# Kernel tuning notes

Measured on AMD Instinct MI355X. Metric: run time of the kernel, lower is better.

Reference implementation:

```python
import jax, jax.numpy as jnp
import numpy as np


def setup_inputs() -> dict:
    key = jax.random.key(0)
    k1, k2, k3 = jax.random.split(key, 3)
    B, C, H, W = 8, 256, 64, 64
    l = jax.random.normal(k1, (B, C, H, W), dtype=jnp.float32)
    # 1x1 conv weights [out=C//2, in=C]; scale 1/sqrt(C) so projected features have ~unit variance
    scale = 1.0 / np.sqrt(C)
    w_theta = jax.random.normal(k2, (C // 2, C), dtype=jnp.float32) * scale
    w_phi = jax.random.normal(k3, (C // 2, C), dtype=jnp.float32) * scale
    return {"l": l, "w_theta": w_theta, "w_phi": w_phi}


def reference(l, w_theta, w_phi):
    # NonLocalOp forward with embed=True, softmax=True
    B, C, H, W = l.shape
    E = w_theta.shape[0]  # C // 2
    HW = H * W
    # 1x1 convs == per-pixel linear maps
    theta = jnp.einsum('bchw,ec->behw', l, w_theta).reshape(B, E, HW)  # [B,E,HW]
    phi = jnp.einsum('bchw,ec->behw', l, w_phi).reshape(B, E, HW)      # [B,E,HW]
    g = l.reshape(B, C, HW)                                            # [B,C,HW]
    # scores: theta^T phi over embed channels, scaled by sqrt(C//2)
    scale = 1.0 / jnp.sqrt(jnp.asarray(C // 2, dtype=l.dtype))
    f = jnp.einsum('beq,bek->bqk', theta, phi) * scale                 # [B,HW,HW]
    f = jax.nn.softmax(f, axis=-1)
    out = jnp.einsum('bqk,bck->bcq', f, g).reshape(B, C, H, W)
    return out
```

## Files before the change

kernel.cpp:

```cpp
#include <hip/hip_runtime.h>
#include <stdint.h>

#define NB 8
#define NC 256
#define NE 128
#define NHW 4096

typedef __bf16 v8bf __attribute__((ext_vector_type(8)));
typedef float v4f __attribute__((ext_vector_type(4)));
typedef float v16f __attribute__((ext_vector_type(16)));
typedef unsigned int v4u __attribute__((ext_vector_type(4)));

typedef unsigned int __attribute__((address_space(1))) uint_g;
typedef unsigned int __attribute__((address_space(3))) uint_l;

#if __has_builtin(__builtin_amdgcn_exp2f)
#define EXP2F(x) __builtin_amdgcn_exp2f(x)
#else
#define EXP2F(x) exp2f(x)
#endif

#define BARRIER_LDS() asm volatile("s_waitcnt lgkmcnt(0)\n\ts_barrier" ::: "memory")
#define WAIT_VM0()    asm volatile("s_waitcnt vmcnt(0)" ::: "memory")

__device__ __forceinline__ void dma16(const unsigned short* g, unsigned short* l) {
    __builtin_amdgcn_global_load_lds((const uint_g*)g, (uint_l*)l, 16, 0, 0);
}

__device__ __forceinline__ unsigned short f2bf(float x) {
    union { float f; unsigned int u; } v; v.f = x;
    unsigned int r = v.u + 0x7fffu + ((v.u >> 16) & 1u);
    return (unsigned short)(r >> 16);
}

__device__ __forceinline__ unsigned int pack_bf2_ru(float a, float b) {
    union { float f; unsigned int u; } va, vb; va.f = a; vb.f = b;
    return ((va.u + 0x8000u) >> 16) | ((vb.u + 0x8000u) & 0xffff0000u);
}

__global__ __launch_bounds__(256) void cast_w_kernel(const float* __restrict__ wt,
                                                     const float* __restrict__ wp,
                                                     unsigned short* __restrict__ Wbf) {
    int i = blockIdx.x * 256 + threadIdx.x;
    const float QS = 0.08838834764831845f * 1.4426950408889634f;
    float v = (i < 32768) ? wt[i] * QS : wp[i - 32768];
    Wbf[i] = f2bf(v);
}

__global__ __launch_bounds__(256, 2) void proj_kernel(const float* __restrict__ l,
                                                      const unsigned short* __restrict__ Wbf,
                                                      unsigned short* __restrict__ Qbf,
                                                      unsigned short* __restrict__ Kbf,
                                                      unsigned short* __restrict__ Vbf) {
    __shared__ __align__(16) unsigned short A[64][264];
    __shared__ __align__(16) unsigned short Ost[2][32][136];
    const int tid = threadIdx.x;
    const int b = blockIdx.x & 7;
    const int qt = (blockIdx.x >> 3) << 6;
    const float* lb = l + ((size_t)b * NC * NHW + qt);

    for (int s = 0; s < 16; ++s) {
        int f = tid + s * 256;
        int c = f >> 4, j = f & 15;
        float4 v = *(const float4*)(lb + (size_t)c * NHW + j * 4);
        ushort4 o4;
        o4.x = f2bf(v.x); o4.y = f2bf(v.y); o4.z = f2bf(v.z); o4.w = f2bf(v.w);
        A[j * 4 + 0][c] = o4.x;
        A[j * 4 + 1][c] = o4.y;
        A[j * 4 + 2][c] = o4.z;
        A[j * 4 + 3][c] = o4.w;
        *(ushort4*)(Vbf + (size_t)b * NC * NHW + (size_t)c * NHW + qt + j * 4) = o4;
    }
    __syncthreads();

    const int w = tid >> 6, L = tid & 63;
    const int l15 = L & 15, q4 = L >> 4;
    const v4f vz = {0.f, 0.f, 0.f, 0.f};
    v4f acc[4][4];
    for (int mt = 0; mt < 4; ++mt)
        for (int nt = 0; nt < 4; ++nt) acc[mt][nt] = vz;

    for (int kf = 0; kf < 8; ++kf) {
        int kc = kf * 32 + q4 * 8;
        v8bf a[4], bb[4];
        for (int mt = 0; mt < 4; ++mt)
            a[mt] = *(const v8bf*)&A[mt * 16 + l15][kc];
        for (int nt = 0; nt < 4; ++nt)
            bb[nt] = *(const v8bf*)(Wbf + (w * 64 + nt * 16 + l15) * 256 + kc);
        for (int mt = 0; mt < 4; ++mt)
            for (int nt = 0; nt < 4; ++nt)
                acc[mt][nt] = __builtin_amdgcn_mfma_f32_16x16x32_bf16(a[mt], bb[nt], acc[mt][nt], 0, 0, 0);
    }

    const int side = w >> 1;
    const int ebase = (w & 1) * 64;
#pragma unroll
    for (int ph = 0; ph < 2; ++ph) {
        __syncthreads();
#pragma unroll
        for (int mh = 0; mh < 2; ++mh) {
            int mt = ph * 2 + mh;
#pragma unroll
            for (int nt = 0; nt < 4; ++nt)
#pragma unroll
                for (int r = 0; r < 4; ++r) {
                    int q32 = mh * 16 + q4 * 4 + r;
                    Ost[side][q32][ebase + nt * 16 + l15] = f2bf(acc[mt][nt][r]);
                }
        }
        __syncthreads();
#pragma unroll
        for (int s = 0; s < 4; ++s) {
            int idx = tid + s * 256;
            int sd = idx >> 9, rem = idx & 511;
            int r32 = rem >> 4, c8 = rem & 15;
            unsigned short* dst = sd ? Kbf : Qbf;
            int c8s = sd ? (c8 ^ (r32 & 15)) : c8;
            *(uint4*)(dst + ((size_t)b * NHW + qt + ph * 32 + r32) * NE + c8s * 8) =
                *(const uint4*)&Ost[sd][r32][c8 * 8];
        }
    }
}

__global__ __launch_bounds__(512, 2) void attn_kernel(const unsigned short* __restrict__ Qbf,
                                                      const unsigned short* __restrict__ Kbf,
                                                      const unsigned short* __restrict__ Vbf,
                                                      float* __restrict__ out) {
    __shared__ __align__(16) unsigned char smem[66048];
    unsigned short* KuS = (unsigned short*)smem;
    unsigned short* PuS = (unsigned short*)(smem + 32768);
    float* lsumF = (float*)(smem + 65536);

    const int tid = threadIdx.x;
    const int b = blockIdx.x & 7;
    const int q128 = (blockIdx.x >> 3) << 7;
    const int w = tid >> 6;
    const int L = tid & 63;
    const int l31 = L & 31, hi = L >> 5;
    const int x15 = l31 & 15;

    const unsigned short* Kb = Kbf + (size_t)b * NHW * NE;
    const unsigned short* Vb = Vbf + (size_t)b * NC * NHW;

    v16f o[2][4];
#pragma unroll
    for (int ct = 0; ct < 2; ++ct)
#pragma unroll
        for (int qt = 0; qt < 4; ++qt)
#pragma unroll
            for (int r = 0; r < 16; ++r) o[ct][qt][r] = 0.f;
    float lacc = 0.f;

    v8bf bq[8];
    v8bf av[2][4];
    const unsigned short* vb0 = nullptr;
    const unsigned short* vb1 = nullptr;

    if (w < 4) {
        const unsigned short* qrow = Qbf + ((size_t)b * NHW + q128 + w * 32 + l31) * NE + hi * 8;
#pragma unroll
        for (int ef = 0; ef < 8; ++ef)
            bq[ef] = *(const v8bf*)(qrow + ef * 16);
#pragma unroll
        for (int jj = 0; jj < 4; ++jj) {
            int j = w * 4 + jj;
            dma16(Kb + (size_t)j * 512 + L * 8, KuS + j * 512);
        }
        WAIT_VM0();
    } else {
        int ci = w - 4;
        vb0 = Vb + (size_t)(ci * 64 + l31) * NHW + hi * 8;
        vb1 = Vb + (size_t)(ci * 64 + 32 + l31) * NHW + hi * 8;
#pragma unroll
        for (int kf = 0; kf < 4; ++kf) {
            av[0][kf] = *(const v8bf*)(vb0 + kf * 16);
            av[1][kf] = *(const v8bf*)(vb1 + kf * 16);
        }
    }
    BARRIER_LDS();

    for (int it = 0; it < 65; ++it) {
        if (w < 4 && it < 64) {
            const int buf = it & 1;
            const int nbuf = (it + 1) & 1;
            const size_t ktn = (size_t)((it + 1) & 63) * 64;
#pragma unroll
            for (int jj = 0; jj < 4; ++jj) {
                int j = w * 4 + jj;
                dma16(Kb + ktn * NE + (size_t)j * 512 + L * 8, KuS + nbuf * 8192 + j * 512);
            }
            const unsigned short* kub = KuS + buf * 8192;
#pragma unroll
            for (int kt = 0; kt < 2; ++kt) {
                v16f sa, sb;
#pragma unroll
                for (int r = 0; r < 16; ++r) { sa[r] = 0.f; sb[r] = 0.f; }
                const unsigned short* krow = kub + (kt * 32 + l31) * 128;
#pragma unroll
                for (int ef = 0; ef < 4; ++ef) {
                    v8bf ak0 = *(const v8bf*)(krow + (((2 * ef + hi) ^ x15) * 8));
                    v8bf ak1 = *(const v8bf*)(krow + (((2 * (ef + 4) + hi) ^ x15) * 8));
                    sa = __builtin_amdgcn_mfma_f32_32x32x16_bf16(ak0, bq[ef], sa, 0, 0, 0);
                    sb = __builtin_amdgcn_mfma_f32_32x32x16_bf16(ak1, bq[ef + 4], sb, 0, 0, 0);
                }
                float p[16];
#pragma unroll
                for (int r = 0; r < 16; ++r) p[r] = EXP2F(sa[r] + sb[r]);
#pragma unroll
                for (int r = 0; r < 16; ++r) lacc += p[r];
                unsigned int pk[8], px[8];
#pragma unroll
                for (int t = 0; t < 8; ++t) pk[t] = pack_bf2_ru(p[2 * t], p[2 * t + 1]);
#pragma unroll
                for (int t = 0; t < 8; ++t) px[t] = (unsigned int)__shfl_xor((int)pk[t], 32);
                union { v4u u; v8bf bb; } f0, f1;
                if (hi == 0) {
                    f0.u = (v4u){pk[0], pk[1], px[0], px[1]};
                    f1.u = (v4u){pk[4], pk[5], px[4], px[5]};
                } else {
                    f0.u = (v4u){px[2], px[3], pk[2], pk[3]};
                    f1.u = (v4u){px[6], px[7], pk[6], pk[7]};
                }
                unsigned short* pw_ = PuS + buf * 8192 + (w * 4 + kt * 2) * 512 + (hi * 32 + l31) * 8;
                *(v4u*)pw_ = f0.u;
                *(v4u*)(pw_ + 512) = f1.u;
            }
            WAIT_VM0();
        }
        if (w >= 4 && it > 0) {
            const int pbuf = (it - 1) & 1;
            const unsigned short* pb = PuS + pbuf * 8192 + (hi * 32 + l31) * 8;
#pragma unroll
            for (int qt = 0; qt < 4; ++qt) {
                v8bf bp[4];
#pragma unroll
                for (int kf = 0; kf < 4; ++kf)
                    bp[kf] = *(const v8bf*)(pb + (qt * 4 + kf) * 512);
#pragma unroll
                for (int kf = 0; kf < 4; ++kf) {
                    o[0][qt] = __builtin_amdgcn_mfma_f32_32x32x16_bf16(av[0][kf], bp[kf], o[0][qt], 0, 0, 0);
                    o[1][qt] = __builtin_amdgcn_mfma_f32_32x32x16_bf16(av[1][kf], bp[kf], o[1][qt], 0, 0, 0);
                }
            }
            const size_t kc0 = (size_t)(it & 63) * 64;
#pragma unroll
            for (int kf = 0; kf < 4; ++kf) {
                av[0][kf] = *(const v8bf*)(vb0 + kc0 + kf * 16);
                av[1][kf] = *(const v8bf*)(vb1 + kc0 + kf * 16);
            }
        }
        BARRIER_LDS();
    }

    if (w < 4) {
        float tot = lacc + __shfl_xor(lacc, 32);
        if (hi == 0) lsumF[w * 32 + l31] = tot;
    }
    BARRIER_LDS();
    if (w >= 4) {
        const int ci = w - 4;
        float inv[4];
#pragma unroll
        for (int qt = 0; qt < 4; ++qt) inv[qt] = 1.0f / lsumF[qt * 32 + l31];
#pragma unroll
        for (int ct = 0; ct < 2; ++ct)
#pragma unroll
            for (int qt = 0; qt < 4; ++qt) {
                float* ob = out + (size_t)b * NC * NHW + q128 + qt * 32 + l31;
#pragma unroll
                for (int r = 0; r < 16; ++r) {
                    int c = ci * 64 + ct * 32 + (r & 3) + 8 * (r >> 2) + 4 * hi;
                    ob[(size_t)c * NHW] = o[ct][qt][r] * inv[qt];
                }
            }
    }
}

extern "C" void kernel_launch(void* const* d_in, const int* in_sizes, int n_in,
                              void* d_out, int out_size, void* d_ws, size_t ws_size,
                              hipStream_t stream) {
    const float* l  = (const float*)d_in[0];
    const float* wt = (const float*)d_in[1];
    const float* wp = (const float*)d_in[2];
    float* out = (float*)d_out;

    char* ws = (char*)d_ws;
    unsigned short* Wbf = (unsigned short*)ws;
    unsigned short* Qbf = (unsigned short*)(ws + 131072);
    unsigned short* Kbf = (unsigned short*)(ws + 131072 + 8388608);
    unsigned short* Vbf = (unsigned short*)(ws + 131072 + 16777216);

    hipLaunchKernelGGL(cast_w_kernel, dim3(256), dim3(256), 0, stream, wt, wp, Wbf);
    hipLaunchKernelGGL(proj_kernel,   dim3(512), dim3(256), 0, stream, l, Wbf, Qbf, Kbf, Vbf);
    hipLaunchKernelGGL(attn_kernel,   dim3(256), dim3(512), 0, stream, Qbf, Kbf, Vbf, out);
}
```

Baseline: 218.1 us.

## Halve attention query tile to 64 with 4-wave blocks and swapped wave roles

Reshapes the attention kernel from 512-thread blocks over 128 queries to 256-thread blocks over 64 queries, doubling the grid to 512 blocks. Two waves now compute scores and softmax probabilities while two waves each accumulate 128 output channels, and alternate blocks swap which wave slots take which role. The aim is better load balance across CUs and less LDS per block, at the cost of reading K and V twice as often per query and more accumulator registers in the PV waves.

After: 506.2 us. +132.1%, slower.

```diff
diff --git a/kernel.cpp b/kernel.cpp
--- a/kernel.cpp
+++ b/kernel.cpp
@@ -122,71 +122,72 @@
     }
 }
 
-__global__ __launch_bounds__(512, 2) void attn_kernel(const unsigned short* __restrict__ Qbf,
+__global__ __launch_bounds__(256, 2) void attn_kernel(const unsigned short* __restrict__ Qbf,
                                                       const unsigned short* __restrict__ Kbf,
                                                       const unsigned short* __restrict__ Vbf,
                                                       float* __restrict__ out) {
-    __shared__ __align__(16) unsigned char smem[66048];
+    __shared__ __align__(16) unsigned char smem[49408];
     unsigned short* KuS = (unsigned short*)smem;
     unsigned short* PuS = (unsigned short*)(smem + 32768);
-    float* lsumF = (float*)(smem + 65536);
+    float* lsumF = (float*)(smem + 49152);
 
     const int tid = threadIdx.x;
     const int b = blockIdx.x & 7;
-    const int q128 = (blockIdx.x >> 3) << 7;
+    const int qt64 = (blockIdx.x >> 3) << 6;
     const int w = tid >> 6;
     const int L = tid & 63;
     const int l31 = L & 31, hi = L >> 5;
     const int x15 = l31 & 15;
+    const int rw = w ^ (((blockIdx.x >> 8) & 1) << 1);
+    const bool isP = rw < 2;
+    const int pi = rw & 1;
 
     const unsigned short* Kb = Kbf + (size_t)b * NHW * NE;
     const unsigned short* Vb = Vbf + (size_t)b * NC * NHW;
 
-    v16f o[2][4];
-#pragma unroll
-    for (int ct = 0; ct < 2; ++ct)
-#pragma unroll
-        for (int qt = 0; qt < 4; ++qt)
+    v16f o[4][2];
+#pragma unroll
+    for (int ct = 0; ct < 4; ++ct)
+#pragma unroll
+        for (int qt = 0; qt < 2; ++qt)
 #pragma unroll
             for (int r = 0; r < 16; ++r) o[ct][qt][r] = 0.f;
     float lacc = 0.f;
 
     v8bf bq[8];
-    v8bf av[2][4];
-    const unsigned short* vb0 = nullptr;
-    const unsigned short* vb1 = nullptr;
-
-    if (w < 4) {
-        const unsigned short* qrow = Qbf + ((size_t)b * NHW + q128 + w * 32 + l31) * NE + hi * 8;
+    v8bf av[4][4];
+    const unsigned short* vbase[4];
+
+    if (isP) {
+        const unsigned short* qrow = Qbf + ((size_t)b * NHW + qt64 + pi * 32 + l31) * NE + hi * 8;
 #pragma unroll
         for (int ef = 0; ef < 8; ++ef)
             bq[ef] = *(const v8bf*)(qrow + ef * 16);
 #pragma unroll
-        for (int jj = 0; jj < 4; ++jj) {
-            int j = w * 4 + jj;
+        for (int jj = 0; jj < 8; ++jj) {
+            int j = pi * 8 + jj;
             dma16(Kb + (size_t)j * 512 + L * 8, KuS + j * 512);
         }
         WAIT_VM0();
     } else {
-        int ci = w - 4;
-        vb0 = Vb + (size_t)(ci * 64 + l31) * NHW + hi * 8;
-        vb1 = Vb + (size_t)(ci * 64 + 32 + l31) * NHW + hi * 8;
-#pragma unroll
-        for (int kf = 0; kf < 4; ++kf) {
-            av[0][kf] = *(const v8bf*)(vb0 + kf * 16);
-            av[1][kf] = *(const v8bf*)(vb1 + kf * 16);
+#pragma unroll
+        for (int ct = 0; ct < 4; ++ct) {
+            vbase[ct] = Vb + (size_t)(pi * 128 + ct * 32 + l31) * NHW + hi * 8;
+#pragma unroll
+            for (int kf = 0; kf < 4; ++kf)
+                av[ct][kf] = *(const v8bf*)(vbase[ct] + kf * 16);
         }
     }
     BARRIER_LDS();
 
     for (int it = 0; it < 65; ++it) {
-        if (w < 4 && it < 64) {
+        if (isP && it < 64) {
             const int buf = it & 1;
             const int nbuf = (it + 1) & 1;
             const size_t ktn = (size_t)((it + 1) & 63) * 64;
 #pragma unroll
-            for (int jj = 0; jj < 4; ++jj) {
-                int j = w * 4 + jj;
+            for (int jj = 0; jj < 8; ++jj) {
+                int j = pi * 8 + jj;
                 dma16(Kb + ktn * NE + (size_t)j * 512 + L * 8, KuS + nbuf * 8192 + j * 512);
             }
             const unsigned short* kub = KuS + buf * 8192;
@@ -221,55 +222,54 @@
                     f0.u = (v4u){px[2], px[3], pk[2], pk[3]};
                     f1.u = (v4u){px[6], px[7], pk[6], pk[7]};
                 }
-                unsigned short* pw_ = PuS + buf * 8192 + (w * 4 + kt * 2) * 512 + (hi * 32 + l31) * 8;
+                unsigned short* pw_ = PuS + buf * 4096 + (pi * 4 + kt * 2) * 512 + (hi * 32 + l31) * 8;
                 *(v4u*)pw_ = f0.u;
                 *(v4u*)(pw_ + 512) = f1.u;
             }
             WAIT_VM0();
         }
-        if (w >= 4 && it > 0) {
+        if (!isP && it > 0) {
             const int pbuf = (it - 1) & 1;
-            const unsigned short* pb = PuS + pbuf * 8192 + (hi * 32 + l31) * 8;
-#pragma unroll
-            for (int qt = 0; qt < 4; ++qt) {
+            const unsigned short* pb = PuS + pbuf * 4096 + (hi * 32 + l31) * 8;
+#pragma unroll
+            for (int qt = 0; qt < 2; ++qt) {
                 v8bf bp[4];
 #pragma unroll
                 for (int kf = 0; kf < 4; ++kf)
                     bp[kf] = *(const v8bf*)(pb + (qt * 4 + kf) * 512);
 #pragma unroll
-                for (int kf = 0; kf < 4; ++kf) {
-                    o[0][qt] = __builtin_amdgcn_mfma_f32_32x32x16_bf16(av[0][kf], bp[kf], o[0][qt], 0, 0, 0);
-                    o[1][qt] = __builtin_amdgcn_mfma_f32_32x32x16_bf16(av[1][kf], bp[kf], o[1][qt], 0, 0, 0);
-                }
+                for (int kf = 0; kf < 4; ++kf)
+#pragma unroll
+                    for (int ct = 0; ct < 4; ++ct)
+                        o[ct][qt] = __builtin_amdgcn_mfma_f32_32x32x16_bf16(av[ct][kf], bp[kf], o[ct][qt], 0, 0, 0);
             }
             const size_t kc0 = (size_t)(it & 63) * 64;
 #pragma unroll
-            for (int kf = 0; kf < 4; ++kf) {
-                av[0][kf] = *(const v8bf*)(vb0 + kc0 + kf * 16);
-                av[1][kf] = *(const v8bf*)(vb1 + kc0 + kf * 16);
-            }
+            for (int ct = 0; ct < 4; ++ct)
+#pragma unroll
+                for (int kf = 0; kf < 4; ++kf)
+                    av[ct][kf] = *(const v8bf*)(vbase[ct] + kc0 + kf * 16);
         }
         BARRIER_LDS();
     }
 
-    if (w < 4) {
+    if (isP) {
         float tot = lacc + __shfl_xor(lacc, 32);
-        if (hi == 0) lsumF[w * 32 + l31] = tot;
+        if (hi == 0) lsumF[pi * 32 + l31] = tot;
     }
     BARRIER_LDS();
-    if (w >= 4) {
-        const int ci = w - 4;
-        float inv[4];
-#pragma unroll
-        for (int qt = 0; qt < 4; ++qt) inv[qt] = 1.0f / lsumF[qt * 32 + l31];
-#pragma unroll
-        for (int ct = 0; ct < 2; ++ct)
-#pragma unroll
-            for (int qt = 0; qt < 4; ++qt) {
-                float* ob = out + (size_t)b * NC * NHW + q128 + qt * 32 + l31;
+    if (!isP) {
+        float inv[2];
+#pragma unroll
+        for (int qt = 0; qt < 2; ++qt) inv[qt] = 1.0f / lsumF[qt * 32 + l31];
+#pragma unroll
+        for (int ct = 0; ct < 4; ++ct)
+#pragma unroll
+            for (int qt = 0; qt < 2; ++qt) {
+                float* ob = out + (size_t)b * NC * NHW + qt64 + qt * 32 + l31;
 #pragma unroll
                 for (int r = 0; r < 16; ++r) {
-                    int c = ci * 64 + ct * 32 + (r & 3) + 8 * (r >> 2) + 4 * hi;
+                    int c = pi * 128 + ct * 32 + (r & 3) + 8 * (r >> 2) + 4 * hi;
                     ob[(size_t)c * NHW] = o[ct][qt][r] * inv[qt];
                 }
             }
@@ -292,5 +292,5 @@
 
     hipLaunchKernelGGL(cast_w_kernel, dim3(256), dim3(256), 0, stream, wt, wp, Wbf);
     hipLaunchKernelGGL(proj_kernel,   dim3(512), dim3(256), 0, stream, l, Wbf, Qbf, Kbf, Vbf);
-    hipLaunchKernelGGL(attn_kernel,   dim3(256), dim3(512), 0, stream, Qbf, Kbf, Vbf, out);
-}
+    hipLaunchKernelGGL(attn_kernel,   dim3(512), dim3(256), 0, stream, Qbf, Kbf, Vbf, out);
+}
```
